# Performance work log

Hardware: AMD Instinct MI355X
Metric: run time of the kernel (lower is better)

## Reference

```python
import jax, jax.numpy as jnp
import numpy as np

D = 256; NH = 8; HD = 32; NL = 4; NP = 4; DFF = 1024; B = 2; LT = 20
SHAPES = [(100, 152), (50, 76), (25, 38), (13, 19)]
LQ = sum(h * w for h, w in SHAPES)  # 20197
LSI = np.cumsum([0] + [h * w for h, w in SHAPES])[:-1].tolist()
EPS = 1e-5


def layer_norm(x, g, b):
    m = jnp.mean(x, -1, keepdims=True)
    v = jnp.mean((x - m) ** 2, -1, keepdims=True)
    return (x - m) * jax.lax.rsqrt(v + EPS) * g + b


def msdeform_core(value, shapes, starts, loc, attn_w):
    # value: [B, Len, NH, HD]; loc: [B, Lq, NH, NL, NP, 2] in [0,1]; attn_w: [B, Lq, NH, NL, NP]
    Bv, _, nH, hd = value.shape
    Lq = loc.shape[1]
    out = jnp.zeros((Bv, Lq, nH, hd), value.dtype)
    for l, (Hl, Wl) in enumerate(shapes):
        s = starts[l]
        vf = value[:, s:s + Hl * Wl]  # [B, Hl*Wl, NH, HD]
        ll = loc[:, :, :, l]          # [B, Lq, NH, NP, 2]
        # grid_sample align_corners=False convention: pix = loc*size - 0.5
        x = ll[..., 0] * Wl - 0.5
        y = ll[..., 1] * Hl - 0.5
        x0 = jnp.floor(x); y0 = jnp.floor(y)
        lx = x - x0; ly = y - y0
        x0i = x0.astype(jnp.int32); y0i = y0.astype(jnp.int32)
        acc = jnp.zeros((Bv, Lq, nH, NP, hd), value.dtype)
        corners = [(0, 0, (1 - lx) * (1 - ly)), (0, 1, lx * (1 - ly)),
                   (1, 0, (1 - lx) * ly), (1, 1, lx * ly)]
        for dy, dx, w in corners:
            xi = x0i + dx; yi = y0i + dy
            valid = (xi >= 0) & (xi < Wl) & (yi >= 0) & (yi < Hl)
            idx = jnp.clip(yi, 0, Hl - 1) * Wl + jnp.clip(xi, 0, Wl - 1)  # [B,Lq,NH,NP]
            idx2 = idx.transpose(0, 1, 3, 2).reshape(Bv, Lq * NP, nH)[..., None]
            g = jnp.take_along_axis(vf, idx2, axis=1)  # [B, Lq*NP, NH, HD]
            g = g.reshape(Bv, Lq, NP, nH, hd).transpose(0, 1, 3, 2, 4)
            acc = acc + g * (w * valid.astype(value.dtype))[..., None]
        out = out + jnp.sum(acc * attn_w[:, :, :, l][..., None], axis=3)
    return out.reshape(Bv, Lq, nH * hd)


def setup_inputs():
    key = jax.random.key(0)
    ks = jax.random.split(key, 40)
    i = [0]
    def nrm(shape, s=0.02):
        i[0] += 1
        return jax.random.normal(ks[i[0]], shape, jnp.float32) * s
    inp = {}
    inp['src'] = nrm((B, LQ, D), 1.0)
    inp['pos'] = nrm((B, LQ, D), 1.0)
    inp['reference_points'] = jax.random.uniform(ks[30], (B, LQ, NL, 2), jnp.float32)
    inp['spatial_shapes'] = jnp.array(SHAPES, jnp.int32)
    inp['level_start_index'] = jnp.array(LSI, jnp.int32)
    inp['text_memory'] = nrm((B, LT, D), 1.0)
    inp['text_mask'] = jnp.zeros((B, LT), bool)
    # MSDeformAttn params
    inp['so_w'] = nrm((NH * NL * NP * 2, D)); inp['so_b'] = nrm((NH * NL * NP * 2,))
    inp['aw_w'] = nrm((NH * NL * NP, D));     inp['aw_b'] = nrm((NH * NL * NP,))
    inp['vp_w'] = nrm((D, D)); inp['vp_b'] = nrm((D,))
    inp['op_w'] = nrm((D, D)); inp['op_b'] = nrm((D,))
    inp['ln1_g'] = jnp.ones((D,)); inp['ln1_b'] = jnp.zeros((D,))
    # cross MHA params
    inp['in_proj_w'] = nrm((3 * D, D)); inp['in_proj_b'] = nrm((3 * D,))
    inp['mha_out_w'] = nrm((D, D));     inp['mha_out_b'] = nrm((D,))
    inp['ln3_g'] = jnp.ones((D,)); inp['ln3_b'] = jnp.zeros((D,))
    # FFN params
    inp['l1_w'] = nrm((DFF, D)); inp['l1_b'] = nrm((DFF,))
    inp['l2_w'] = nrm((D, DFF)); inp['l2_b'] = nrm((D,))
    inp['ln2_g'] = jnp.ones((D,)); inp['ln2_b'] = jnp.zeros((D,))
    return inp


def reference(src, pos, reference_points, spatial_shapes, level_start_index, text_memory, text_mask,
              so_w, so_b, aw_w, aw_b, vp_w, vp_b, op_w, op_b, ln1_g, ln1_b,
              in_proj_w, in_proj_b, mha_out_w, mha_out_b, ln3_g, ln3_b,
              l1_w, l1_b, l2_w, l2_b, ln2_g, ln2_b):
    shapes = [tuple(r) for r in np.asarray(jax.device_get(spatial_shapes)).tolist()]
    starts = np.asarray(jax.device_get(level_start_index)).tolist()
    Bv, Lq, _ = src.shape
    q = src + pos
    # --- MSDeformAttn ---
    value = (src @ vp_w.T + vp_b).reshape(Bv, Lq, NH, HD)
    offs = (q @ so_w.T + so_b).reshape(Bv, Lq, NH, NL, NP, 2)
    aw = jax.nn.softmax((q @ aw_w.T + aw_b).reshape(Bv, Lq, NH, NL * NP), axis=-1)
    aw = aw.reshape(Bv, Lq, NH, NL, NP)
    # offset normalizer is (W, H) per level
    normalizer = jnp.array([[w, h] for (h, w) in shapes], src.dtype)  # [NL, 2]
    loc = reference_points[:, :, None, :, None, :] + offs / normalizer[None, None, None, :, None, :]
    ms = msdeform_core(value, shapes, starts, loc, aw) @ op_w.T + op_b
    x = layer_norm(src + ms, ln1_g, ln1_b)
    # --- cross MHA (query = x+pos, key = value = text_memory) ---
    wq, wk, wv = in_proj_w[:D], in_proj_w[D:2 * D], in_proj_w[2 * D:]
    bq, bk, bv = in_proj_b[:D], in_proj_b[D:2 * D], in_proj_b[2 * D:]
    qh = ((x + pos) @ wq.T + bq).reshape(Bv, Lq, NH, HD)
    kh = (text_memory @ wk.T + bk).reshape(Bv, LT, NH, HD)
    vh = (text_memory @ wv.T + bv).reshape(Bv, LT, NH, HD)
    scores = jnp.einsum('bqhd,bkhd->bhqk', qh, kh) / np.sqrt(HD)
    attn = jax.nn.softmax(scores, axis=-1)
    ctx = jnp.einsum('bhqk,bkhd->bqhd', attn, vh).reshape(Bv, Lq, D)
    x = layer_norm(x + (ctx @ mha_out_w.T + mha_out_b), ln3_g, ln3_b)
    # --- FFN ---
    ffn = jax.nn.relu(x @ l1_w.T + l1_b) @ l2_w.T + l2_b
    x = layer_norm(x + ffn, ln2_g, ln2_b)
    return (x, text_memory)
```

## Files before the change

### kernel.cpp

```cpp
#include <hip/hip_runtime.h>
#include <math.h>

#define D     256
#define NH    8
#define HDIM  32
#define NL    4
#define NPT   4
#define DFF   1024
#define BB    2
#define LT    20
#define LQ    20197
#define NROWS (BB*LQ)
#define SFL   ((size_t)NROWS * D)

typedef __attribute__((ext_vector_type(8))) short bf16x8;
typedef __attribute__((ext_vector_type(4))) float f32x4;

__device__ __forceinline__ unsigned short f2b(float f) {
    unsigned int u = __float_as_uint(f);
    unsigned int r = (u + 0x7FFFu + ((u >> 16) & 1u)) >> 16;
    return (unsigned short)r;
}
__device__ __forceinline__ float b2f(unsigned short u) {
    return __uint_as_float((unsigned int)u << 16);
}
__device__ __forceinline__ unsigned int pk2(float a, float b) {
    return (unsigned int)f2b(a) | ((unsigned int)f2b(b) << 16);
}

template<int CTRL>
__device__ __forceinline__ int dppi(int v) {
    return __builtin_amdgcn_update_dpp(0, v, CTRL, 0xF, 0xF, true);
}
template<int CTRL>
__device__ __forceinline__ float dppf(float v) {
    return __uint_as_float((unsigned int)__builtin_amdgcn_update_dpp(
        0, (int)__float_as_uint(v), CTRL, 0xF, 0xF, true));
}

#define GLDS16(g, l) __builtin_amdgcn_global_load_lds( \
    (const __attribute__((address_space(1))) unsigned int*)(g), \
    (__attribute__((address_space(3))) unsigned int*)(l), 16, 0, 0)

__global__ __launch_bounds__(256) void gemm_mfma(const unsigned short* __restrict__ A,
                                                 const unsigned short* __restrict__ W,
                                                 const float* __restrict__ bias,
                                                 float* __restrict__ Cf,
                                                 unsigned short* __restrict__ Cb,
                                                 int M, int Nout, int K, int relu)
{
    __shared__ __align__(16) unsigned short As[128 * 32];
    __shared__ __align__(16) unsigned short Ws[128 * 32];
    const int tid  = threadIdx.x;
    const int wave = tid >> 6, lane = tid & 63;
    const int row0 = blockIdx.x * 128, n0 = blockIdx.y * 128;
    const int wm = (wave >> 1) * 64, wn = (wave & 1) * 64;

    const int srow = (wave << 5) + (lane >> 2);
    const int kcol = (lane & 3) << 3;
    const int ar0 = min(row0 + srow,      M - 1);
    const int ar1 = min(row0 + srow + 16, M - 1);
    const unsigned short* Ap0 = A + (size_t)ar0 * K + kcol;
    const unsigned short* Ap1 = A + (size_t)ar1 * K + kcol;
    const unsigned short* Wp0 = W + (size_t)(n0 + srow) * K + kcol;
    const unsigned short* Wp1 = W + (size_t)(n0 + srow + 16) * K + kcol;
    unsigned short* lA0 = &As[(wave << 10)];
    unsigned short* lA1 = &As[(wave << 10) + 512];
    unsigned short* lW0 = &Ws[(wave << 10)];
    unsigned short* lW1 = &Ws[(wave << 10) + 512];

    f32x4 acc[4][4];
#pragma unroll
    for (int i = 0; i < 4; ++i)
#pragma unroll
        for (int j = 0; j < 4; ++j)
#pragma unroll
            for (int r = 0; r < 4; ++r) acc[i][j][r] = 0.f;

    const int fr = lane & 15;
    const int fk = (lane >> 4) << 3;

    for (int k0 = 0; k0 < K; k0 += 32) {
        GLDS16(Ap0 + k0, lA0);
        GLDS16(Ap1 + k0, lA1);
        GLDS16(Wp0 + k0, lW0);
        GLDS16(Wp1 + k0, lW1);
        __syncthreads();
        bf16x8 af[4], wf[4];
#pragma unroll
        for (int t = 0; t < 4; ++t) {
            af[t] = *(const bf16x8*)&As[(wm + t * 16 + fr) * 32 + fk];
            wf[t] = *(const bf16x8*)&Ws[(wn + t * 16 + fr) * 32 + fk];
        }
#pragma unroll
        for (int i = 0; i < 4; ++i)
#pragma unroll
            for (int j = 0; j < 4; ++j)
                acc[i][j] = __builtin_amdgcn_mfma_f32_16x16x32_bf16(af[i], wf[j], acc[i][j], 0, 0, 0);
        __syncthreads();
    }

    const int rq = (lane >> 4) << 2;
    const int cq = lane & 15;
#pragma unroll
    for (int mt = 0; mt < 4; ++mt) {
#pragma unroll
        for (int r = 0; r < 4; ++r) {
            const int row = row0 + wm + mt * 16 + rq + r;
            if (row < M) {
#pragma unroll
                for (int nt = 0; nt < 4; ++nt) {
                    const int c = n0 + wn + nt * 16 + cq;
                    float v = acc[mt][nt][r] + bias[c];
                    if (relu) v = fmaxf(v, 0.f);
                    if (Cb) Cb[(size_t)row * Nout + c] = f2b(v);
                    else    Cf[(size_t)row * Nout + c] = v;
                }
            }
        }
    }
}

struct W8 {
    const float* s[8];
    unsigned short* d[8];
    int n[8];
};
__global__ __launch_bounds__(256) void cast_w8(W8 w)
{
    const int seg = blockIdx.y;
    const int n = w.n[seg];
    const float* s = w.s[seg];
    unsigned short* d = w.d[seg];
    for (int i = blockIdx.x * 256 + threadIdx.x; i < n; i += gridDim.x * 256)
        d[i] = f2b(s[i]);
}

__global__ __launch_bounds__(384) void cat_bias(const float* __restrict__ sb,
                                                const float* __restrict__ ab,
                                                float* __restrict__ o)
{
    const int t = threadIdx.x;
    o[t] = (t < 256) ? sb[t] : ab[t - 256];
}

__global__ __launch_bounds__(256) void cast_pair(const float4* __restrict__ src,
                                                 const float4* __restrict__ pos,
                                                 ushort4* __restrict__ srcb,
                                                 ushort4* __restrict__ qbf, int n4)
{
    const int i = blockIdx.x * 256 + threadIdx.x;
    if (i < n4) {
        const float4 s = src[i], p = pos[i];
        srcb[i] = make_ushort4(f2b(s.x), f2b(s.y), f2b(s.z), f2b(s.w));
        qbf[i]  = make_ushort4(f2b(s.x + p.x), f2b(s.y + p.y), f2b(s.z + p.z), f2b(s.w + p.w));
    }
}

#define SEL4(a0,a1,a2,a3) (j < 2 ? (j == 0 ? (a0) : (a1)) : (j == 2 ? (a2) : (a3)))

__global__ __launch_bounds__(256) void msdeform(const unsigned short* __restrict__ value,
                                                const float* __restrict__ oa,
                                                const float* __restrict__ refp,
                                                unsigned short* __restrict__ out)
{
    const int tid  = threadIdx.x;
    const int lane = tid & 63;
    const int row  = blockIdx.x * 8 + ((tid >> 6) << 1) + (lane >> 5);
    if (row >= NROWS) return;
    const int b   = row / LQ;
    const int sub = lane & 31;
    const int h   = sub >> 2;
    const int j   = sub & 3;
    const int ch  = (h << 5) + (j << 3);
    const unsigned short* vbase = value + (size_t)b * LQ * D + ch;

    const float* orow = oa + (size_t)row * 384;
    const float4 o0 = *(const float4*)(orow + (h << 5) + (j << 3));
    const float4 o1 = *(const float4*)(orow + (h << 5) + (j << 3) + 4);
    const float oxr[4] = {o0.x, o0.z, o1.x, o1.z};
    const float oyr[4] = {o0.y, o0.w, o1.y, o1.w};
    const float4 lg = *(const float4*)(orow + 256 + (h << 4) + (j << 2));
    float mx = fmaxf(fmaxf(lg.x, lg.y), fmaxf(lg.z, lg.w));
    mx = fmaxf(mx, dppf<0xB1>(mx));
    mx = fmaxf(mx, dppf<0x4E>(mx));
    const float e0 = __expf(lg.x - mx), e1 = __expf(lg.y - mx);
    const float e2 = __expf(lg.z - mx), e3 = __expf(lg.w - mx);
    float sm = e0 + e1 + e2 + e3;
    sm += dppf<0xB1>(sm);
    sm += dppf<0x4E>(sm);
    const float inv = 1.f / sm;
    const float pr[4] = {e0 * inv, e1 * inv, e2 * inv, e3 * inv};

    const int   Wi   = SEL4(152, 76, 38, 19);
    const int   Hi   = SEL4(100, 50, 25, 13);
    const int   st   = SEL4(0, 15200, 19000, 19950);
    const float invW = SEL4(1.f/152.f, 1.f/76.f, 1.f/38.f, 1.f/19.f);
    const float invH = SEL4(1.f/100.f, 1.f/50.f, 1.f/25.f, 1.f/13.f);
    const float Wf = (float)Wi, Hf = (float)Hi;
    const float2 rxy = *(const float2*)(refp + (size_t)row * 8 + (j << 1));

    unsigned int ip[8];
    float wcs[16];
#pragma unroll
    for (int p = 0; p < 4; ++p) {
        const float x = fmaf(oxr[p], invW, rxy.x) * Wf - 0.5f;
        const float y = fmaf(oyr[p], invH, rxy.y) * Hf - 0.5f;
        const float x0f = floorf(x), y0f = floorf(y);
        const float lx = x - x0f, ly = y - y0f;
        const int x0 = (int)x0f, y0 = (int)y0f;
        const int x1 = x0 + 1,  y1 = y0 + 1;
        const float vx0 = (x0 >= 0 && x0 < Wi) ? 1.f : 0.f;
        const float vx1 = (x1 >= 0 && x1 < Wi) ? 1.f : 0.f;
        const float vy0 = (y0 >= 0 && y0 < Hi) ? 1.f : 0.f;
        const float vy1 = (y1 >= 0 && y1 < Hi) ? 1.f : 0.f;
        const int cx0 = min(max(x0, 0), Wi - 1), cx1 = min(max(x1, 0), Wi - 1);
        const int cy0 = min(max(y0, 0), Hi - 1), cy1 = min(max(y1, 0), Hi - 1);
        const float wap = pr[p];
        const float wx0 = (1.f - lx) * vx0,        wx1 = lx * vx1;
        const float wy0 = (1.f - ly) * vy0 * wap,  wy1 = ly * vy1 * wap;
        const int r0 = st + cy0 * Wi, r1 = st + cy1 * Wi;
        ip[2*p]     = (unsigned int)(r0 + cx0) | ((unsigned int)(r0 + cx1) << 16);
        ip[2*p + 1] = (unsigned int)(r1 + cx0) | ((unsigned int)(r1 + cx1) << 16);
        wcs[4*p]     = wx0 * wy0;
        wcs[4*p + 1] = wx1 * wy0;
        wcs[4*p + 2] = wx0 * wy1;
        wcs[4*p + 3] = wx1 * wy1;
    }

    float acc[8] = {0.f,0.f,0.f,0.f,0.f,0.f,0.f,0.f};

#define GATHER(i_, w_) do { \
        const uint4 g_ = *(const uint4*)(vbase + ((size_t)(i_) << 8)); \
        acc[0] = fmaf(w_, __uint_as_float(g_.x << 16),          acc[0]); \
        acc[1] = fmaf(w_, __uint_as_float(g_.x & 0xffff0000u),  acc[1]); \
        acc[2] = fmaf(w_, __uint_as_float(g_.y << 16),          acc[2]); \
        acc[3] = fmaf(w_, __uint_as_float(g_.y & 0xffff0000u),  acc[3]); \
        acc[4] = fmaf(w_, __uint_as_float(g_.z << 16),          acc[4]); \
        acc[5] = fmaf(w_, __uint_as_float(g_.z & 0xffff0000u),  acc[5]); \
        acc[6] = fmaf(w_, __uint_as_float(g_.w << 16),          acc[6]); \
        acc[7] = fmaf(w_, __uint_as_float(g_.w & 0xffff0000u),  acc[7]); \
    } while (0)

#define POINT(L, p) do { \
        const unsigned int pk0_ = (unsigned int)dppi<(L)*85>((int)ip[2*(p)]); \
        const unsigned int pk1_ = (unsigned int)dppi<(L)*85>((int)ip[2*(p)+1]); \
        const float w0_ = dppf<(L)*85>(wcs[4*(p)]); \
        const float w1_ = dppf<(L)*85>(wcs[4*(p)+1]); \
        const float w2_ = dppf<(L)*85>(wcs[4*(p)+2]); \
        const float w3_ = dppf<(L)*85>(wcs[4*(p)+3]); \
        GATHER(pk0_ & 0xffffu, w0_); \
        GATHER(pk0_ >> 16,     w1_); \
        GATHER(pk1_ & 0xffffu, w2_); \
        GATHER(pk1_ >> 16,     w3_); \
    } while (0)

#define LEVEL(L) do { POINT(L,0); POINT(L,1); POINT(L,2); POINT(L,3); } while (0)

    LEVEL(0); LEVEL(1); LEVEL(2); LEVEL(3);

#undef LEVEL
#undef POINT
#undef GATHER

    uint4 o;
    o.x = pk2(acc[0], acc[1]); o.y = pk2(acc[2], acc[3]);
    o.z = pk2(acc[4], acc[5]); o.w = pk2(acc[6], acc[7]);
    *(uint4*)(out + (size_t)row * D + ch) = o;
}

__global__ __launch_bounds__(256) void add_ln(const float* a, const float* b,
                                              const float* __restrict__ g,
                                              const float* __restrict__ be,
                                              const float* __restrict__ pos,
                                              float* out, unsigned short* outb)
{
    const int lane = threadIdx.x & 63;
    const int row  = blockIdx.x * 4 + (threadIdx.x >> 6);
    if (row >= NROWS) return;
    const size_t base = (size_t)row * D + (lane << 2);
    const float4 av = *(const float4*)(a + base);
    const float4 bv = *(const float4*)(b + base);
    float4 v = make_float4(av.x + bv.x, av.y + bv.y, av.z + bv.z, av.w + bv.w);
    float s = v.x + v.y + v.z + v.w;
#pragma unroll
    for (int off = 1; off < 64; off <<= 1) s += __shfl_xor(s, off);
    const float mean = s * (1.f / 256.f);
    const float4 d = make_float4(v.x - mean, v.y - mean, v.z - mean, v.w - mean);
    float q = d.x*d.x + d.y*d.y + d.z*d.z + d.w*d.w;
#pragma unroll
    for (int off = 1; off < 64; off <<= 1) q += __shfl_xor(q, off);
    const float rstd = rsqrtf(q * (1.f / 256.f) + 1e-5f);
    const float4 gv = *(const float4*)(g  + (lane << 2));
    const float4 bev = *(const float4*)(be + (lane << 2));
    float4 o;
    o.x = d.x * rstd * gv.x + bev.x;
    o.y = d.y * rstd * gv.y + bev.y;
    o.z = d.z * rstd * gv.z + bev.z;
    o.w = d.w * rstd * gv.w + bev.w;
    *(float4*)(out + base) = o;
    if (outb) {
        float4 p = make_float4(0.f, 0.f, 0.f, 0.f);
        if (pos) p = *(const float4*)(pos + base);
        uint2 u;
        u.x = pk2(o.x + p.x, o.y + p.y);
        u.y = pk2(o.z + p.z, o.w + p.w);
        *(uint2*)(outb + base) = u;
    }
}

__global__ __launch_bounds__(256) void text_kv(const float* __restrict__ text,
                                               const float* __restrict__ ipw,
                                               const float* __restrict__ ipb,
                                               float* __restrict__ kh,
                                               float* __restrict__ vh,
                                               float* __restrict__ outtxt)
{
    __shared__ float ts[D];
    const int row = blockIdx.x, t = threadIdx.x;
    const float tv = text[(size_t)row * D + t];
    ts[t] = tv;
    outtxt[(size_t)row * D + t] = tv;
    __syncthreads();
    const float* wk = ipw + (size_t)(D + t) * D;
    const float* wv = ipw + (size_t)(2 * D + t) * D;
    float sk = ipb[D + t], sv = ipb[2 * D + t];
    for (int k = 0; k < D; ++k) {
        sk = fmaf(ts[k], wk[k], sk);
        sv = fmaf(ts[k], wv[k], sv);
    }
    kh[(size_t)row * D + t] = sk;
    vh[(size_t)row * D + t] = sv;
}

__global__ __launch_bounds__(256) void text_attn(const float* __restrict__ qh,
                                                 const float* __restrict__ kh,
                                                 const float* __restrict__ vh,
                                                 unsigned short* __restrict__ ctx)
{
    __shared__ float vs[LT * D];
    __shared__ float qs[8][D];
    const int b  = blockIdx.y;
    const int q0 = blockIdx.x * 8;
    const int t  = threadIdx.x;
    const int nr = min(8, LQ - q0);

    {
        const float4* vsrc = (const float4*)(vh + (size_t)b * LT * D);
        float4* vdst = (float4*)vs;
#pragma unroll
        for (int i = 0; i < 5; ++i) vdst[t + 256 * i] = vsrc[t + 256 * i];
        for (int r = 0; r < nr; ++r)
            qs[r][t] = qh[((size_t)b * LQ + q0 + r) * D + t];
    }
    __syncthreads();

    const int h = t >> 5, d = t & 31;
    const int lane = t & 63;
    float kf[32];
    if (d < LT) {
        const float4* kr = (const float4*)(kh + (size_t)(b * LT + d) * D + h * HDIM);
#pragma unroll
        for (int i = 0; i < 8; ++i) {
            const float4 kv = kr[i];
            kf[4*i] = kv.x; kf[4*i+1] = kv.y; kf[4*i+2] = kv.z; kf[4*i+3] = kv.w;
        }
    }
    float vv[LT];
#pragma unroll
    for (int k = 0; k < LT; ++k) vv[k] = vs[k * D + t];

    for (int r = 0; r < nr; ++r) {
        float sc = -1e30f;
        if (d < LT) {
            const float4* qq = (const float4*)(qs[r] + h * HDIM);
            float s = 0.f;
#pragma unroll
            for (int i = 0; i < 8; ++i) {
                const float4 qv = qq[i];
                s = fmaf(qv.x, kf[4*i],   s); s = fmaf(qv.y, kf[4*i+1], s);
                s = fmaf(qv.z, kf[4*i+2], s); s = fmaf(qv.w, kf[4*i+3], s);
            }
            sc = s * 0.17677669529663687f;
        }
        float mx = sc;
#pragma unroll
        for (int off = 1; off < 32; off <<= 1) mx = fmaxf(mx, __shfl_xor(mx, off));
        const float e = (d < LT) ? __expf(sc - mx) : 0.f;
        float sm = e;
#pragma unroll
        for (int off = 1; off < 32; off <<= 1) sm += __shfl_xor(sm, off);
        const float pr = e * (1.f / sm);
        float o0 = 0.f, o1 = 0.f;
#pragma unroll
        for (int k = 0; k < LT; k += 2) {
            const float p0 = __shfl(pr, (lane & 32) | k);
            const float p1 = __shfl(pr, (lane & 32) | (k + 1));
            o0 = fmaf(p0, vv[k],     o0);
            o1 = fmaf(p1, vv[k + 1], o1);
        }
        ctx[((size_t)b * LQ + q0 + r) * D + t] = f2b(o0 + o1);
    }
}

extern "C" void kernel_launch(void* const* d_in, const int* in_sizes, int n_in,
                              void* d_out, int out_size, void* d_ws, size_t ws_size,
                              hipStream_t stream)
{
    const float* src  = (const float*)d_in[0];
    const float* pos  = (const float*)d_in[1];
    const float* refp = (const float*)d_in[2];
    const float* text = (const float*)d_in[5];
    const float* so_w = (const float*)d_in[7];
    const float* so_b = (const float*)d_in[8];
    const float* aw_w = (const float*)d_in[9];
    const float* aw_b = (const float*)d_in[10];
    const float* vp_w = (const float*)d_in[11];
    const float* vp_b = (const float*)d_in[12];
    const float* op_w = (const float*)d_in[13];
    const float* op_b = (const float*)d_in[14];
    const float* ln1g = (const float*)d_in[15];
    const float* ln1b = (const float*)d_in[16];
    const float* ipw  = (const float*)d_in[17];
    const float* ipb  = (const float*)d_in[18];
    const float* mow  = (const float*)d_in[19];
    const float* mob  = (const float*)d_in[20];
    const float* ln3g = (const float*)d_in[21];
    const float* ln3b = (const float*)d_in[22];
    const float* l1w  = (const float*)d_in[23];
    const float* l1b  = (const float*)d_in[24];
    const float* l2w  = (const float*)d_in[25];
    const float* l2b  = (const float*)d_in[26];
    const float* ln2g = (const float*)d_in[27];
    const float* ln2b = (const float*)d_in[28];

    float* ws = (float*)d_ws;
    float*          oa     = ws;
    unsigned short* srcb   = (unsigned short*)(ws + SFL + SFL / 2);
    unsigned short* mscb   = srcb;
    unsigned short* qbf    = (unsigned short*)(ws + 2 * SFL);
    unsigned short* valb   = (unsigned short*)(ws + 2 * SFL + SFL / 2);
    float*          gen32  = ws + 3 * SFL;
    float*          x12    = ws + 4 * SFL;
    unsigned short* wb     = (unsigned short*)(ws + 5 * SFL);
    unsigned short* hidden = (unsigned short*)ws;

    unsigned short* wb_vp = wb;
    unsigned short* wb_so = wb + 65536;
    unsigned short* wb_aw = wb + 131072;
    unsigned short* wb_op = wb + 163840;
    unsigned short* wb_wq = wb + 229376;
    unsigned short* wb_mo = wb + 294912;
    unsigned short* wb_l1 = wb + 360448;
    unsigned short* wb_l2 = wb + 622592;
    float* kvk  = ws + 5 * SFL + 442368;
    float* kvv  = kvk + (size_t)BB * LT * D;
    float* sobc = kvv + (size_t)BB * LT * D;

    const int M = NROWS;
    const int gx = (M + 127) / 128;
    const dim3 blk(256);
    const int n4 = (int)(SFL / 4);
    const int vgrid = (n4 + 255) / 256;
    const int dgrid = (M + 7) / 8;
    const int lgrid = (M + 3) / 4;

    W8 w8;
    w8.s[0] = vp_w; w8.d[0] = wb_vp; w8.n[0] = 65536;
    w8.s[1] = so_w; w8.d[1] = wb_so; w8.n[1] = 65536;
    w8.s[2] = aw_w; w8.d[2] = wb_aw; w8.n[2] = 32768;
    w8.s[3] = op_w; w8.d[3] = wb_op; w8.n[3] = 65536;
    w8.s[4] = ipw;  w8.d[4] = wb_wq; w8.n[4] = 65536;
    w8.s[5] = mow;  w8.d[5] = wb_mo; w8.n[5] = 65536;
    w8.s[6] = l1w;  w8.d[6] = wb_l1; w8.n[6] = 262144;
    w8.s[7] = l2w;  w8.d[7] = wb_l2; w8.n[7] = 262144;
    cast_w8<<<dim3(128, 8), blk, 0, stream>>>(w8);
    cat_bias<<<dim3(1), dim3(384), 0, stream>>>(so_b, aw_b, sobc);
    cast_pair<<<dim3(vgrid), blk, 0, stream>>>((const float4*)src, (const float4*)pos,
                                               (ushort4*)srcb, (ushort4*)qbf, n4);
    gemm_mfma<<<dim3(gx, 2), blk, 0, stream>>>(srcb, wb_vp, vp_b, nullptr, valb, M, 256, 256, 0);
    gemm_mfma<<<dim3(gx, 3), blk, 0, stream>>>(qbf, wb_so, sobc, oa, nullptr, M, 384, 256, 0);
    msdeform<<<dim3(dgrid), blk, 0, stream>>>(valb, oa, refp, mscb);
    gemm_mfma<<<dim3(gx, 2), blk, 0, stream>>>(mscb, wb_op, op_b, gen32, nullptr, M, 256, 256, 0);
    add_ln<<<dim3(lgrid), blk, 0, stream>>>(src, gen32, ln1g, ln1b, pos, x12, qbf);
    float* outx = (float*)d_out;
    text_kv<<<dim3(BB * LT), blk, 0, stream>>>(text, ipw, ipb, kvk, kvv, outx + SFL);
    gemm_mfma<<<dim3(gx, 2), blk, 0, stream>>>(qbf, wb_wq, ipb, gen32, nullptr, M, 256, 256, 0);
    text_attn<<<dim3((LQ + 7) / 8, BB), blk, 0, stream>>>(gen32, kvk, kvv, qbf);
    gemm_mfma<<<dim3(gx, 2), blk, 0, stream>>>(qbf, wb_mo, mob, gen32, nullptr, M, 256, 256, 0);
    add_ln<<<dim3(lgrid), blk, 0, stream>>>(x12, gen32, ln3g, ln3b, nullptr, x12, qbf);
    gemm_mfma<<<dim3(gx, 8), blk, 0, stream>>>(qbf, wb_l1, l1b, nullptr, hidden, M, 1024, 256, 1);
    gemm_mfma<<<dim3(gx, 2), blk, 0, stream>>>(hidden, wb_l2, l2b, outx, nullptr, M, 256, 1024, 0);
    add_ln<<<dim3(lgrid), blk, 0, stream>>>(x12, outx, ln2g, ln2b, nullptr, outx, nullptr);
}
```

Before: 680.7 us.

## Fuse output-projection GEMMs with residual add and LayerNorm epilogue

Adds a gemm_ln kernel in which each 512-thread block computes a full 128x256 output row tile, so the residual add, bias and LayerNorm can run in the epilogue using a cross-wave shared-memory reduction of sum and sum of squares. It replaces the three gemm_mfma plus add_ln pairs, removing the fp32 intermediate round trip and three kernel launches. In exchange the grid is half as large per GEMM, since N is no longer split. Variance is computed as E[x^2]-mean^2, which is less numerically robust. The kernel writes x12 in place while reading it as the residual, which is safe only because each element is read before it is written by the same thread.

```diff
diff --git a/kernel.cpp b/kernel.cpp
--- a/kernel.cpp
+++ b/kernel.cpp
@@ -115,6 +115,128 @@
                     if (relu) v = fmaxf(v, 0.f);
                     if (Cb) Cb[(size_t)row * Nout + c] = f2b(v);
                     else    Cf[(size_t)row * Nout + c] = v;
+                }
+            }
+        }
+    }
+}
+
+__global__ __launch_bounds__(512, 4) void gemm_ln(const unsigned short* __restrict__ A,
+                                                  const unsigned short* __restrict__ W,
+                                                  const float* __restrict__ bias,
+                                                  const float* __restrict__ res,
+                                                  const float* __restrict__ pos,
+                                                  const float* __restrict__ lng,
+                                                  const float* __restrict__ lnb,
+                                                  float* __restrict__ out,
+                                                  unsigned short* __restrict__ outb,
+                                                  int M, int K)
+{
+    __shared__ __align__(16) unsigned short As[128 * 32];
+    __shared__ __align__(16) unsigned short Ws[256 * 32];
+    const int tid  = threadIdx.x;
+    const int w    = tid >> 6, lane = tid & 63;
+    const int row0 = blockIdx.x * 128;
+    const int wm   = (w & 3) << 5;
+    const int wn2  = (w >> 2) << 7;
+
+    const int srow = lane >> 2;
+    const int kcol = (lane & 3) << 3;
+    const int arow = min(row0 + (w << 4) + srow, M - 1);
+    const unsigned short* Ap  = A + (size_t)arow * K + kcol;
+    const unsigned short* Wp0 = W + (size_t)((w << 5) + srow) * K + kcol;
+    const unsigned short* Wp1 = W + (size_t)((w << 5) + 16 + srow) * K + kcol;
+    unsigned short* lA  = &As[(w << 4) * 32];
+    unsigned short* lW0 = &Ws[(w << 5) * 32];
+    unsigned short* lW1 = &Ws[((w << 5) + 16) * 32];
+
+    f32x4 acc[2][8];
+#pragma unroll
+    for (int i = 0; i < 2; ++i)
+#pragma unroll
+        for (int j = 0; j < 8; ++j)
+#pragma unroll
+            for (int r = 0; r < 4; ++r) acc[i][j][r] = 0.f;
+
+    const int fr = lane & 15;
+    const int fk = (lane >> 4) << 3;
+
+    for (int k0 = 0; k0 < K; k0 += 32) {
+        GLDS16(Ap + k0, lA);
+        GLDS16(Wp0 + k0, lW0);
+        GLDS16(Wp1 + k0, lW1);
+        __syncthreads();
+        const bf16x8 af0 = *(const bf16x8*)&As[(wm + fr) * 32 + fk];
+        const bf16x8 af1 = *(const bf16x8*)&As[(wm + 16 + fr) * 32 + fk];
+#pragma unroll
+        for (int nt = 0; nt < 8; ++nt) {
+            const bf16x8 wf = *(const bf16x8*)&Ws[(wn2 + nt * 16 + fr) * 32 + fk];
+            acc[0][nt] = __builtin_amdgcn_mfma_f32_16x16x32_bf16(wf, af0, acc[0][nt], 0, 0, 0);
+            acc[1][nt] = __builtin_amdgcn_mfma_f32_16x16x32_bf16(wf, af1, acc[1][nt], 0, 0, 0);
+        }
+        __syncthreads();
+    }
+
+    const int cq = lane & 15;
+    const int rq = (lane >> 4) << 2;
+    float2* red = (float2*)As;
+
+#pragma unroll
+    for (int mt = 0; mt < 2; ++mt) {
+        const int m_g = row0 + wm + mt * 16 + cq;
+        float s = 0.f, q = 0.f;
+#pragma unroll
+        for (int nt = 0; nt < 8; ++nt) {
+            const int c4 = wn2 + nt * 16 + rq;
+            const float4 bb = *(const float4*)(bias + c4);
+            float4 rr = make_float4(0.f, 0.f, 0.f, 0.f);
+            if (m_g < M) rr = *(const float4*)(res + (size_t)m_g * D + c4);
+            acc[mt][nt][0] += bb.x + rr.x;
+            acc[mt][nt][1] += bb.y + rr.y;
+            acc[mt][nt][2] += bb.z + rr.z;
+            acc[mt][nt][3] += bb.w + rr.w;
+#pragma unroll
+            for (int r = 0; r < 4; ++r) {
+                const float v = acc[mt][nt][r];
+                s += v; q += v * v;
+            }
+        }
+        s += __shfl_xor(s, 16); s += __shfl_xor(s, 32);
+        q += __shfl_xor(q, 16); q += __shfl_xor(q, 32);
+        if (lane < 16)
+            red[(((wm + mt * 16 + lane) << 1) | (w >> 2))] = make_float2(s, q);
+    }
+    __syncthreads();
+
+#pragma unroll
+    for (int mt = 0; mt < 2; ++mt) {
+        const int ml  = wm + mt * 16 + cq;
+        const int m_g = row0 + ml;
+        const float2 h0 = red[(ml << 1)];
+        const float2 h1 = red[(ml << 1) | 1];
+        const float S = h0.x + h1.x, Q = h0.y + h1.y;
+        const float mean = S * (1.f / 256.f);
+        const float var  = Q * (1.f / 256.f) - mean * mean;
+        const float rstd = rsqrtf(var + 1e-5f);
+        if (m_g < M) {
+#pragma unroll
+            for (int nt = 0; nt < 8; ++nt) {
+                const int c4 = wn2 + nt * 16 + rq;
+                const float4 gg = *(const float4*)(lng + c4);
+                const float4 ee = *(const float4*)(lnb + c4);
+                float4 o;
+                o.x = (acc[mt][nt][0] - mean) * rstd * gg.x + ee.x;
+                o.y = (acc[mt][nt][1] - mean) * rstd * gg.y + ee.y;
+                o.z = (acc[mt][nt][2] - mean) * rstd * gg.z + ee.z;
+                o.w = (acc[mt][nt][3] - mean) * rstd * gg.w + ee.w;
+                *(float4*)(out + (size_t)m_g * D + c4) = o;
+                if (outb) {
+                    float4 p = make_float4(0.f, 0.f, 0.f, 0.f);
+                    if (pos) p = *(const float4*)(pos + (size_t)m_g * D + c4);
+                    uint2 u;
+                    u.x = pk2(o.x + p.x, o.y + p.y);
+                    u.y = pk2(o.z + p.z, o.w + p.w);
+                    *(uint2*)(outb + (size_t)m_g * D + c4) = u;
                 }
             }
         }
@@ -267,46 +389,6 @@
     o.x = pk2(acc[0], acc[1]); o.y = pk2(acc[2], acc[3]);
     o.z = pk2(acc[4], acc[5]); o.w = pk2(acc[6], acc[7]);
     *(uint4*)(out + (size_t)row * D + ch) = o;
-}
-
-__global__ __launch_bounds__(256) void add_ln(const float* a, const float* b,
-                                              const float* __restrict__ g,
-                                              const float* __restrict__ be,
-                                              const float* __restrict__ pos,
-                                              float* out, unsigned short* outb)
-{
-    const int lane = threadIdx.x & 63;
-    const int row  = blockIdx.x * 4 + (threadIdx.x >> 6);
-    if (row >= NROWS) return;
-    const size_t base = (size_t)row * D + (lane << 2);
-    const float4 av = *(const float4*)(a + base);
-    const float4 bv = *(const float4*)(b + base);
-    float4 v = make_float4(av.x + bv.x, av.y + bv.y, av.z + bv.z, av.w + bv.w);
-    float s = v.x + v.y + v.z + v.w;
-#pragma unroll
-    for (int off = 1; off < 64; off <<= 1) s += __shfl_xor(s, off);
-    const float mean = s * (1.f / 256.f);
-    const float4 d = make_float4(v.x - mean, v.y - mean, v.z - mean, v.w - mean);
-    float q = d.x*d.x + d.y*d.y + d.z*d.z + d.w*d.w;
-#pragma unroll
-    for (int off = 1; off < 64; off <<= 1) q += __shfl_xor(q, off);
-    const float rstd = rsqrtf(q * (1.f / 256.f) + 1e-5f);
-    const float4 gv = *(const float4*)(g  + (lane << 2));
-    const float4 bev = *(const float4*)(be + (lane << 2));
-    float4 o;
-    o.x = d.x * rstd * gv.x + bev.x;
-    o.y = d.y * rstd * gv.y + bev.y;
-    o.z = d.z * rstd * gv.z + bev.z;
-    o.w = d.w * rstd * gv.w + bev.w;
-    *(float4*)(out + base) = o;
-    if (outb) {
-        float4 p = make_float4(0.f, 0.f, 0.f, 0.f);
-        if (pos) p = *(const float4*)(pos + base);
-        uint2 u;
-        u.x = pk2(o.x + p.x, o.y + p.y);
-        u.y = pk2(o.z + p.z, o.w + p.w);
-        *(uint2*)(outb + base) = u;
-    }
 }
 
 __global__ __launch_bounds__(256) void text_kv(const float* __restrict__ text,
@@ -463,7 +545,6 @@
     const int n4 = (int)(SFL / 4);
     const int vgrid = (n4 + 255) / 256;
     const int dgrid = (M + 7) / 8;
-    const int lgrid = (M + 3) / 4;
 
     W8 w8;
     w8.s[0] = vp_w; w8.d[0] = wb_vp; w8.n[0] = 65536;
@@ -481,15 +562,15 @@
     gemm_mfma<<<dim3(gx, 2), blk, 0, stream>>>(srcb, wb_vp, vp_b, nullptr, valb, M, 256, 256, 0);
     gemm_mfma<<<dim3(gx, 3), blk, 0, stream>>>(qbf, wb_so, sobc, oa, nullptr, M, 384, 256, 0);
     msdeform<<<dim3(dgrid), blk, 0, stream>>>(valb, oa, refp, mscb);
-    gemm_mfma<<<dim3(gx, 2), blk, 0, stream>>>(mscb, wb_op, op_b, gen32, nullptr, M, 256, 256, 0);
-    add_ln<<<dim3(lgrid), blk, 0, stream>>>(src, gen32, ln1g, ln1b, pos, x12, qbf);
+    gemm_ln<<<dim3(gx), dim3(512), 0, stream>>>(mscb, wb_op, op_b, src, pos,
+                                                ln1g, ln1b, x12, qbf, M, 256);
     float* outx = (float*)d_out;
     text_kv<<<dim3(BB * LT), blk, 0, stream>>>(text, ipw, ipb, kvk, kvv, outx + SFL);
     gemm_mfma<<<dim3(gx, 2), blk, 0, stream>>>(qbf, wb_wq, ipb, gen32, nullptr, M, 256, 256, 0);
     text_attn<<<dim3((LQ + 7) / 8, BB), blk, 0, stream>>>(gen32, kvk, kvv, qbf);
-    gemm_mfma<<<dim3(gx, 2), blk, 0, stream>>>(qbf, wb_mo, mob, gen32, nullptr, M, 256, 256, 0);
-    add_ln<<<dim3(lgrid), blk, 0, stream>>>(x12, gen32, ln3g, ln3b, nullptr, x12, qbf);
+    gemm_ln<<<dim3(gx), dim3(512), 0, stream>>>(qbf, wb_mo, mob, x12, nullptr,
+                                                ln3g, ln3b, x12, qbf, M, 256);
     gemm_mfma<<<dim3(gx, 8), blk, 0, stream>>>(qbf, wb_l1, l1b, nullptr, hidden, M, 1024, 256, 1);
-    gemm_mfma<<<dim3(gx, 2), blk, 0, stream>>>(hidden, wb_l2, l2b, outx, nullptr, M, 256, 1024, 0);
-    add_ln<<<dim3(lgrid), blk, 0, stream>>>(x12, outx, ln2g, ln2b, nullptr, outx, nullptr);
-}
+    gemm_ln<<<dim3(gx), dim3(512), 0, stream>>>(hidden, wb_l2, l2b, x12, nullptr,
+                                                ln2g, ln2b, outx, nullptr, M, 1024);
+}
```

New measurement: 712.6 us. 1.05x slower.

## Double-buffer LDS tiles in MFMA GEMM to overlap loads with compute

Applied to the files above, without the earlier changes.

Turns the GEMM's single LDS tile into two buffers. The next K-slice is prefetched with global_load_lds while MFMAs run on the current slice, and the per-iteration barrier count drops from two to one. The goal is to hide global memory latency behind matrix math. In exchange, LDS use per block doubles, which may reduce occupancy.

```diff
diff --git a/kernel.cpp b/kernel.cpp
--- a/kernel.cpp
+++ b/kernel.cpp
@@ -49,8 +49,8 @@
                                                  unsigned short* __restrict__ Cb,
                                                  int M, int Nout, int K, int relu)
 {
-    __shared__ __align__(16) unsigned short As[128 * 32];
-    __shared__ __align__(16) unsigned short Ws[128 * 32];
+    __shared__ __align__(16) unsigned short As[2][128 * 32];
+    __shared__ __align__(16) unsigned short Ws[2][128 * 32];
     const int tid  = threadIdx.x;
     const int wave = tid >> 6, lane = tid & 63;
     const int row0 = blockIdx.x * 128, n0 = blockIdx.y * 128;
@@ -64,10 +64,8 @@
     const unsigned short* Ap1 = A + (size_t)ar1 * K + kcol;
     const unsigned short* Wp0 = W + (size_t)(n0 + srow) * K + kcol;
     const unsigned short* Wp1 = W + (size_t)(n0 + srow + 16) * K + kcol;
-    unsigned short* lA0 = &As[(wave << 10)];
-    unsigned short* lA1 = &As[(wave << 10) + 512];
-    unsigned short* lW0 = &Ws[(wave << 10)];
-    unsigned short* lW1 = &Ws[(wave << 10) + 512];
+    const int aoff0 = (wave << 10);
+    const int aoff1 = (wave << 10) + 512;
 
     f32x4 acc[4][4];
 #pragma unroll
@@ -80,17 +78,27 @@
     const int fr = lane & 15;
     const int fk = (lane >> 4) << 3;
 
-    for (int k0 = 0; k0 < K; k0 += 32) {
-        GLDS16(Ap0 + k0, lA0);
-        GLDS16(Ap1 + k0, lA1);
-        GLDS16(Wp0 + k0, lW0);
-        GLDS16(Wp1 + k0, lW1);
-        __syncthreads();
+    GLDS16(Ap0, &As[0][aoff0]);
+    GLDS16(Ap1, &As[0][aoff1]);
+    GLDS16(Wp0, &Ws[0][aoff0]);
+    GLDS16(Wp1, &Ws[0][aoff1]);
+    __syncthreads();
+
+    const int nt = K >> 5;
+    int cur = 0;
+    for (int t = 0; t < nt; ++t) {
+        if (t + 1 < nt) {
+            const int k1 = (t + 1) << 5;
+            GLDS16(Ap0 + k1, &As[cur ^ 1][aoff0]);
+            GLDS16(Ap1 + k1, &As[cur ^ 1][aoff1]);
+            GLDS16(Wp0 + k1, &Ws[cur ^ 1][aoff0]);
+            GLDS16(Wp1 + k1, &Ws[cur ^ 1][aoff1]);
+        }
         bf16x8 af[4], wf[4];
 #pragma unroll
-        for (int t = 0; t < 4; ++t) {
-            af[t] = *(const bf16x8*)&As[(wm + t * 16 + fr) * 32 + fk];
-            wf[t] = *(const bf16x8*)&Ws[(wn + t * 16 + fr) * 32 + fk];
+        for (int t4 = 0; t4 < 4; ++t4) {
+            af[t4] = *(const bf16x8*)&As[cur][(wm + t4 * 16 + fr) * 32 + fk];
+            wf[t4] = *(const bf16x8*)&Ws[cur][(wn + t4 * 16 + fr) * 32 + fk];
         }
 #pragma unroll
         for (int i = 0; i < 4; ++i)
@@ -98,6 +106,7 @@
             for (int j = 0; j < 4; ++j)
                 acc[i][j] = __builtin_amdgcn_mfma_f32_16x16x32_bf16(af[i], wf[j], acc[i][j], 0, 0, 0);
         __syncthreads();
+        cur ^= 1;
     }
 
     const int rq = (lane >> 4) << 2;
@@ -109,9 +118,9 @@
             const int row = row0 + wm + mt * 16 + rq + r;
             if (row < M) {
 #pragma unroll
-                for (int nt = 0; nt < 4; ++nt) {
-                    const int c = n0 + wn + nt * 16 + cq;
-                    float v = acc[mt][nt][r] + bias[c];
+                for (int nt2 = 0; nt2 < 4; ++nt2) {
+                    const int c = n0 + wn + nt2 * 16 + cq;
+                    float v = acc[mt][nt2][r] + bias[c];
                     if (relu) v = fmaxf(v, 0.f);
                     if (Cb) Cb[(size_t)row * Nout + c] = f2b(v);
                     else    Cf[(size_t)row * Nout + c] = v;
```

New measurement: 682.8 us. About the same (+0.3%).
